# Kernel tuning notes

Measured on AMD Instinct MI355X. Metric: run time of the kernel, lower is better.

Reference implementation:

```python
import jax, jax.numpy as jnp
import numpy as np

H, N, CH, RANK = 512, 64, 1, 1
SEQ_L = 4096


def setup_inputs() -> dict:
    key = jax.random.key(0)
    k0, k1, k2, k3, k4 = jax.random.split(key, 5)
    # A = -exp(A_real) + i*A_imag  (real_transform='exp'); HiPPO-style imag init
    A_real = jnp.log(0.5 + jax.random.uniform(k0, (H, N), dtype=jnp.float32))
    A_imag = jnp.broadcast_to(np.pi * jnp.arange(N, dtype=jnp.float32), (H, N)).copy()
    # complex params stored as (..., 2) real/imag pairs (torch.view_as_real layout)
    B = (0.5 ** 0.5) * jax.random.normal(k1, (1, H, N, 2), dtype=jnp.float32)
    C = jax.random.normal(k2, (CH, H, N, 2), dtype=jnp.float32)
    P = (0.5 ** 0.5) * jax.random.normal(k3, (RANK, H, N, 2), dtype=jnp.float32)
    # dt = exp(inv_dt) log-uniform in [1e-3, 1e-1]  (dt_transform='exp')
    lo, hi = np.log(1e-3), np.log(1e-1)
    inv_dt = (lo + (hi - lo) * jax.random.uniform(k4, (H,), dtype=jnp.float32)).astype(jnp.float32)
    return {"A_real": A_real, "A_imag": A_imag, "B": B, "C": C, "P": P,
            "inv_dt": inv_dt, "L": SEQ_L}


def _c(x):
    # view_as_complex
    return x[..., 0] + 1j * x[..., 1]


def _s4_kernel(A_real, A_imag, B, C, P, inv_dt, L):
    dt = jnp.exp(inv_dt)                       # (H,)
    A = -jnp.exp(A_real) + 1j * A_imag          # (H, N) complex64
    Bc, Cc, Pc = _c(B), _c(C), _c(P)            # (1,H,N), (CH,H,N), (R,H,N)
    Q = jnp.conj(Pc)

    Lf = L // 2 + 1
    omega = jnp.exp(-2j * jnp.pi / L) ** jnp.arange(Lf)   # FFT nodes, (Lf,)
    z = 2 * (1 - omega) / (1 + omega)                      # bilinear-transform freqs

    A_dt = A * dt[:, None]                     # (H, N)
    Bcat = jnp.concatenate([Bc, Pc], axis=0)   # (1+R, H, N)
    Ccat = jnp.concatenate([Cc, Q], axis=0)    # (CH+R, H, N)
    v = Bcat[:, None] * Ccat[None]             # (1+R, CH+R, H, N)
    v = v * dt[:, None]

    # Cauchy kernel with implicit conjugate-pair symmetry:
    #   r[a,b,h,l] = sum_n v/(z - A_dt) + conj(v)/(z - conj(A_dt))
    denom = 1.0 / (z - A_dt[..., None])                    # (H, N, Lf)
    r = jnp.einsum('abhn,hnl->abhl', v, denom)
    denom_c = 1.0 / (z - jnp.conj(A_dt)[..., None])
    r = r + jnp.einsum('abhn,hnl->abhl', jnp.conj(v), denom_c)

    # rank-1 Woodbury correction
    k_f = r[:-1, :-1] - r[:-1, -1:] * r[-1:, :-1] / (1 + r[-1:, -1:])
    k_f = k_f * 2 / (1 + omega)

    k = jnp.fft.irfft(k_f, n=L)                # (1, CH, H, L) real
    k = k[..., :L]
    return k[-1]                               # k_B: (CH, H, L)


def reference(A_real, A_imag, B, C, P, inv_dt, L):
    return _s4_kernel(A_real, A_imag, B, C, P, inv_dt, L)
```

## Files before the change

kernel.cpp:

```cpp
#include <hip/hip_runtime.h>
#include <math.h>

namespace {
constexpr int kH = 512;
constexpr int kN = 64;
constexpr int kL = 4096;
constexpr int kM = 2048;
constexpr int kRec = 20;
constexpr int kThreads = 256;
constexpr int kFftThreads = 512;
constexpr float kPi = 3.14159265358979323846f;
}

__device__ __forceinline__ int lpad(int i) { return i + (i >> 4); }

__global__ __launch_bounds__(64)
void s4_prep(const float* __restrict__ A_real, const float* __restrict__ A_imag,
             const float* __restrict__ Bv, const float* __restrict__ Cv,
             const float* __restrict__ Pv, const float* __restrict__ inv_dt,
             float* __restrict__ cst)
{
    const int h = blockIdx.x;
    const int n = threadIdx.x;
    const int idx = h * kN + n;
    const float dt = expf(inv_dt[h]);
    const float ar = -expf(A_real[idx]) * dt;
    const float ai =  A_imag[idx] * dt;
    const float br = Bv[idx*2+0], bi = Bv[idx*2+1];
    const float cr = Cv[idx*2+0], ci = Cv[idx*2+1];
    const float pr = Pv[idx*2+0], pi = Pv[idx*2+1];
    const float v00r = (br*cr - bi*ci)*dt, v00i = (br*ci + bi*cr)*dt;
    const float v01r = (br*pr + bi*pi)*dt, v01i = (bi*pr - br*pi)*dt;
    const float v10r = (pr*cr - pi*ci)*dt, v10i = (pr*ci + pi*cr)*dt;
    const float v11r = (pr*pr + pi*pi)*dt;
    const float ar2 = ar*ar;
    const float C1  = ar2 + ai*ai;
    const float dd  = ar2 - ai*ai;

    float* r = cst + idx * kRec;
    r[0]  = ai;  r[1] = ar2;
    r[2]  = -2.f*C1*(v00r*ar + v00i*ai);  r[3]  = 2.f*(v00i*ai - v00r*ar);
    r[4]  = -4.f*v00r*dd - 8.f*v00i*ar*ai; r[5]  = -4.f*v00r;
    r[6]  = -2.f*C1*(v01r*ar + v01i*ai);  r[7]  = 2.f*(v01i*ai - v01r*ar);
    r[8]  = -4.f*v01r*dd - 8.f*v01i*ar*ai; r[9]  = -4.f*v01r;
    r[10] = -2.f*C1*(v10r*ar + v10i*ai);  r[11] = 2.f*(v10i*ai - v10r*ar);
    r[12] = -4.f*v10r*dd - 8.f*v10i*ar*ai; r[13] = -4.f*v10r;
    r[14] = -2.f*C1*(v11r*ar);            r[15] = -2.f*v11r*ar;
    r[16] = -4.f*v11r*dd;                 r[17] = -4.f*v11r;
    r[18] = 0.f; r[19] = 0.f;
}

__global__ __launch_bounds__(kThreads)
void s4_spectrum(const float* __restrict__ cst, float2* __restrict__ Xg)
{
    const int h   = blockIdx.x >> 2;
    const int q   = blockIdx.x & 3;
    const int tid = threadIdx.x;
    const int la  = q * 512 + tid;

    float tv[2], t2v[2], sv[2];
    #pragma unroll
    for (int b = 0; b < 2; ++b) {
        const int l = la + 256 * b;
        float sn, cn;
        sincosf((float)l * (kPi / (float)kL), &sn, &cn);
        tv[b]  = sn / cn;
        t2v[b] = 2.f * tv[b];
        sv[b]  = t2v[b] * t2v[b];
    }

    float A0[2][4] = {{0,0,0,0},{0,0,0,0}};
    float A1[2][4] = {{0,0,0,0},{0,0,0,0}};
    float B0[2][4] = {{0,0,0,0},{0,0,0,0}};
    float B1[2][4] = {{0,0,0,0},{0,0,0,0}};

    const float* rec = cst + (size_t)h * kN * kRec;
    #pragma unroll 1
    for (int n0 = 0; n0 < kN; n0 += 4) {
        float rr[4][18];
        #pragma unroll
        for (int j = 0; j < 4; ++j) {
            const float* r = rec + (n0 + j) * kRec;
            #pragma unroll
            for (int k = 0; k < 18; ++k) rr[j][k] = r[k];
        }
        #pragma unroll
        for (int j = 0; j < 4; ++j) {
            const float ai = rr[j][0], ar2 = rr[j][1];
            #pragma unroll
            for (int b = 0; b < 2; ++b) {
                const float w1 = t2v[b] - ai, w2 = t2v[b] + ai;
                const float m1 = fmaf(w1, w1, ar2), m2 = fmaf(w2, w2, ar2);
                const float invD = __builtin_amdgcn_rcpf(m1 * m2);
                #pragma unroll
                for (int p = 0; p < 4; ++p) {
                    A0[b][p] = fmaf(rr[j][2 + 4*p], invD, A0[b][p]);
                    A1[b][p] = fmaf(rr[j][3 + 4*p], invD, A1[b][p]);
                    B0[b][p] = fmaf(rr[j][4 + 4*p], invD, B0[b][p]);
                    B1[b][p] = fmaf(rr[j][5 + 4*p], invD, B1[b][p]);
                }
            }
        }
    }

    #pragma unroll
    for (int b = 0; b < 2; ++b) {
        const int l = la + 256 * b;
        const float t = tv[b], s = sv[b];
        const float s00r = fmaf(s, A1[b][0], A0[b][0]);
        const float s00i = t * fmaf(s, B1[b][0], B0[b][0]);
        const float s01r = fmaf(s, A1[b][1], A0[b][1]);
        const float s01i = t * fmaf(s, B1[b][1], B0[b][1]);
        const float s10r = fmaf(s, A1[b][2], A0[b][2]);
        const float s10i = t * fmaf(s, B1[b][2], B0[b][2]);
        const float s11r = fmaf(s, A1[b][3], A0[b][3]);
        const float s11i = t * fmaf(s, B1[b][3], B0[b][3]);
        const float nr = s01r*s10r - s01i*s10i;
        const float ni = s01r*s10i + s01i*s10r;
        const float dr = 1.f + s11r, di = s11i;
        const float qd = __builtin_amdgcn_rcpf(fmaf(dr, dr, di*di));
        const float wr = (nr*dr + ni*di) * qd;
        const float wi = (ni*dr - nr*di) * qd;
        const float gr = s00r - wr, gi = s00i - wi;
        Xg[h*kM + l] = make_float2(fmaf(-gi, t, gr), fmaf(gr, t, gi));
    }
}

__global__ __launch_bounds__(kFftThreads)
void s4_ifft(const float* __restrict__ Bv,
             const float* __restrict__ Cv,
             const float* __restrict__ inv_dt,
             float* __restrict__ out)
{
    __shared__ float2 W2[kM + kM / 16];
    __shared__ float2 TW[kM / 2 + kM / 32];
    __shared__ float  XnyqR;

    const int h   = blockIdx.x;
    const int tid = threadIdx.x;
    const float2* Xg = (const float2*)(out + (size_t)h * kL);

    if (tid < kN) {
        const int idx = h * kN + tid;
        const float dt = expf(inv_dt[h]);
        const float br = Bv[idx*2+0], bi = Bv[idx*2+1];
        const float cr = Cv[idx*2+0], ci = Cv[idx*2+1];
        float vr = (br*cr - bi*ci) * dt;
        #pragma unroll
        for (int off = 32; off > 0; off >>= 1) vr += __shfl_down(vr, off, 64);
        if (tid == 0) XnyqR = vr;
    }
    for (int j = tid; j < kM / 2; j += kFftThreads) {
        float s, c;
        sincosf((2.0f * kPi / (float)kM) * (float)j, &s, &c);
        TW[lpad(j)] = make_float2(c, s);
    }
    __syncthreads();

    for (int k = tid; k <= kM / 2; k += kFftThreads) {
        const float2 Xa = Xg[k];
        const float2 Xb = (k == 0) ? make_float2(XnyqR, 0.0f) : Xg[kM - k];
        const float Er = 0.5f * (Xa.x + Xb.x);
        const float Ei = 0.5f * (Xa.y - Xb.y);
        const float Dr = 0.5f * (Xa.x - Xb.x);
        const float Di = 0.5f * (Xa.y + Xb.y);
        float s, c;
        sincosf((2.0f * kPi / (float)kL) * (float)k, &s, &c);
        const float Or = c * Dr - s * Di;
        const float Oi = c * Di + s * Dr;
        const int rk = (int)(__brev((unsigned)k) >> 21);
        W2[lpad(rk)] = make_float2(Er - Oi, Ei + Or);
        if (k != 0 && k != kM / 2) {
            const int rmk = (int)(__brev((unsigned)(kM - k)) >> 21);
            W2[lpad(rmk)] = make_float2(Er + Oi, Or - Ei);
        }
    }
    __syncthreads();

    for (int hs = 1; hs < kM; hs <<= 1) {
        const int tw_stride = (kM / 2) / hs;
        for (int j = tid; j < kM / 2; j += kFftThreads) {
            const int pos = j & (hs - 1);
            const int grp = j / hs;
            const int i0  = grp * 2 * hs + pos;
            const int i1  = i0 + hs;
            const float2 tw = TW[lpad(pos * tw_stride)];
            const float2 a = W2[lpad(i0)];
            const float2 b = W2[lpad(i1)];
            const float tr = tw.x * b.x - tw.y * b.y;
            const float ti = tw.x * b.y + tw.y * b.x;
            W2[lpad(i0)] = make_float2(a.x + tr, a.y + ti);
            W2[lpad(i1)] = make_float2(a.x - tr, a.y - ti);
        }
        __syncthreads();
    }

    const float invM = 1.0f / (float)kM;
    float2* out2 = (float2*)(out + (size_t)h * kL);
    for (int n = tid; n < kM; n += kFftThreads) {
        const float2 zn = W2[lpad(n)];
        out2[n] = make_float2(zn.x * invM, zn.y * invM);
    }
}

extern "C" void kernel_launch(void* const* d_in, const int* in_sizes, int n_in,
                              void* d_out, int out_size, void* d_ws, size_t ws_size,
                              hipStream_t stream) {
    const float* A_real = (const float*)d_in[0];
    const float* A_imag = (const float*)d_in[1];
    const float* B      = (const float*)d_in[2];
    const float* C      = (const float*)d_in[3];
    const float* P      = (const float*)d_in[4];
    const float* inv_dt = (const float*)d_in[5];
    float* out = (float*)d_out;

    float* cst = (float*)d_ws;

    s4_prep<<<dim3(kH), dim3(64), 0, stream>>>(A_real, A_imag, B, C, P, inv_dt,
                                               cst);
    s4_spectrum<<<dim3(kH * 4), dim3(kThreads), 0, stream>>>(cst, (float2*)out);
    s4_ifft<<<dim3(kH), dim3(kFftThreads), 0, stream>>>(B, C, inv_dt, out);
}
```

Before: 125.3 us.

## Pack coefficient records in pairs and use packed FP32 FMA in spectrum loop

The prep kernel now interleaves the coefficient records of two adjacent state indices into one 40-float pair record. The spectrum kernel processes two states per iteration using 2-wide vector FMAs (v_pk_fma_f32 on CDNA), keeping dual-lane accumulators and summing the lanes at the end. The aim is to halve the issue count of the dominant FMA accumulation and let the loads be vectorized. The cost is more accumulator registers and a slightly different summation order.

Result: faster. 113.4 us (-9.5%).

```diff
diff --git a/kernel.cpp b/kernel.cpp
--- a/kernel.cpp
+++ b/kernel.cpp
@@ -6,13 +6,18 @@
 constexpr int kN = 64;
 constexpr int kL = 4096;
 constexpr int kM = 2048;
-constexpr int kRec = 20;
+constexpr int kPairRec = 40;
 constexpr int kThreads = 256;
 constexpr int kFftThreads = 512;
 constexpr float kPi = 3.14159265358979323846f;
 }
 
+typedef float v2f __attribute__((ext_vector_type(2)));
+
 __device__ __forceinline__ int lpad(int i) { return i + (i >> 4); }
+__device__ __forceinline__ v2f fma2(v2f a, v2f b, v2f c) {
+    return __builtin_elementwise_fma(a, b, c);
+}
 
 __global__ __launch_bounds__(64)
 void s4_prep(const float* __restrict__ A_real, const float* __restrict__ A_imag,
@@ -37,17 +42,21 @@
     const float C1  = ar2 + ai*ai;
     const float dd  = ar2 - ai*ai;
 
-    float* r = cst + idx * kRec;
-    r[0]  = ai;  r[1] = ar2;
-    r[2]  = -2.f*C1*(v00r*ar + v00i*ai);  r[3]  = 2.f*(v00i*ai - v00r*ar);
-    r[4]  = -4.f*v00r*dd - 8.f*v00i*ar*ai; r[5]  = -4.f*v00r;
-    r[6]  = -2.f*C1*(v01r*ar + v01i*ai);  r[7]  = 2.f*(v01i*ai - v01r*ar);
-    r[8]  = -4.f*v01r*dd - 8.f*v01i*ar*ai; r[9]  = -4.f*v01r;
-    r[10] = -2.f*C1*(v10r*ar + v10i*ai);  r[11] = 2.f*(v10i*ai - v10r*ar);
-    r[12] = -4.f*v10r*dd - 8.f*v10i*ar*ai; r[13] = -4.f*v10r;
-    r[14] = -2.f*C1*(v11r*ar);            r[15] = -2.f*v11r*ar;
-    r[16] = -4.f*v11r*dd;                 r[17] = -4.f*v11r;
-    r[18] = 0.f; r[19] = 0.f;
+    float co[16];
+    co[0]  = -2.f*C1*(v00r*ar + v00i*ai);   co[1]  = 2.f*(v00i*ai - v00r*ar);
+    co[2]  = -4.f*v00r*dd - 8.f*v00i*ar*ai; co[3]  = -4.f*v00r;
+    co[4]  = -2.f*C1*(v01r*ar + v01i*ai);   co[5]  = 2.f*(v01i*ai - v01r*ar);
+    co[6]  = -4.f*v01r*dd - 8.f*v01i*ar*ai; co[7]  = -4.f*v01r;
+    co[8]  = -2.f*C1*(v10r*ar + v10i*ai);   co[9]  = 2.f*(v10i*ai - v10r*ar);
+    co[10] = -4.f*v10r*dd - 8.f*v10i*ar*ai; co[11] = -4.f*v10r;
+    co[12] = -2.f*C1*(v11r*ar);             co[13] = -2.f*v11r*ar;
+    co[14] = -4.f*v11r*dd;                  co[15] = -4.f*v11r;
+
+    float* base = cst + ((size_t)h * (kN/2) + (n >> 1)) * kPairRec + (n & 1);
+    base[0] = ai;
+    base[2] = ar2;
+    #pragma unroll
+    for (int k = 0; k < 16; ++k) base[4 + 2*k] = co[k];
 }
 
 __global__ __launch_bounds__(kThreads)
@@ -58,47 +67,50 @@
     const int tid = threadIdx.x;
     const int la  = q * 512 + tid;
 
-    float tv[2], t2v[2], sv[2];
+    float tv[2], sv[2];
+    v2f t2p[2];
     #pragma unroll
     for (int b = 0; b < 2; ++b) {
         const int l = la + 256 * b;
         float sn, cn;
         sincosf((float)l * (kPi / (float)kL), &sn, &cn);
-        tv[b]  = sn / cn;
-        t2v[b] = 2.f * tv[b];
-        sv[b]  = t2v[b] * t2v[b];
-    }
-
-    float A0[2][4] = {{0,0,0,0},{0,0,0,0}};
-    float A1[2][4] = {{0,0,0,0},{0,0,0,0}};
-    float B0[2][4] = {{0,0,0,0},{0,0,0,0}};
-    float B1[2][4] = {{0,0,0,0},{0,0,0,0}};
-
-    const float* rec = cst + (size_t)h * kN * kRec;
-    #pragma unroll 1
-    for (int n0 = 0; n0 < kN; n0 += 4) {
-        float rr[4][18];
+        tv[b] = sn / cn;
+        const float t2 = 2.f * tv[b];
+        sv[b] = t2 * t2;
+        t2p[b] = (v2f){t2, t2};
+    }
+
+    v2f A0[2][4], A1[2][4], B0[2][4], B1[2][4];
+    #pragma unroll
+    for (int b = 0; b < 2; ++b)
         #pragma unroll
-        for (int j = 0; j < 4; ++j) {
-            const float* r = rec + (n0 + j) * kRec;
+        for (int p = 0; p < 4; ++p) {
+            A0[b][p] = (v2f){0.f, 0.f}; A1[b][p] = (v2f){0.f, 0.f};
+            B0[b][p] = (v2f){0.f, 0.f}; B1[b][p] = (v2f){0.f, 0.f};
+        }
+
+    const v2f* rec = (const v2f*)(cst + (size_t)h * (kN/2) * kPairRec);
+    #pragma unroll 2
+    for (int j = 0; j < kN/2; ++j) {
+        const v2f* r = rec + j * (kPairRec/2);
+        const v2f aip  = r[0];
+        const v2f ar2p = r[1];
+        #pragma unroll
+        for (int b = 0; b < 2; ++b) {
+            const v2f w1 = t2p[b] - aip;
+            const v2f w2 = t2p[b] + aip;
+            const v2f m1 = fma2(w1, w1, ar2p);
+            const v2f m2 = fma2(w2, w2, ar2p);
+            const v2f D  = m1 * m2;
+            v2f qv;
+            qv.x = __builtin_amdgcn_rcpf(D.x);
+            qv.y = __builtin_amdgcn_rcpf(D.y);
             #pragma unroll
-            for (int k = 0; k < 18; ++k) rr[j][k] = r[k];
-        }
-        #pragma unroll
-        for (int j = 0; j < 4; ++j) {
-            const float ai = rr[j][0], ar2 = rr[j][1];
-            #pragma unroll
-            for (int b = 0; b < 2; ++b) {
-                const float w1 = t2v[b] - ai, w2 = t2v[b] + ai;
-                const float m1 = fmaf(w1, w1, ar2), m2 = fmaf(w2, w2, ar2);
-                const float invD = __builtin_amdgcn_rcpf(m1 * m2);
-                #pragma unroll
-                for (int p = 0; p < 4; ++p) {
-                    A0[b][p] = fmaf(rr[j][2 + 4*p], invD, A0[b][p]);
-                    A1[b][p] = fmaf(rr[j][3 + 4*p], invD, A1[b][p]);
-                    B0[b][p] = fmaf(rr[j][4 + 4*p], invD, B0[b][p]);
-                    B1[b][p] = fmaf(rr[j][5 + 4*p], invD, B1[b][p]);
-                }
+            for (int p = 0; p < 4; ++p) {
+                A0[b][p] = fma2(r[2 + 4*p + 0], qv, A0[b][p]);
+                A1[b][p] = fma2(r[2 + 4*p + 1], qv, A1[b][p]);
+                B0[b][p] = fma2(r[2 + 4*p + 2], qv, B0[b][p]);
+                B1[b][p] = fma2(r[2 + 4*p + 3], qv, B1[b][p]);
             }
         }
     }
@@ -106,15 +118,20 @@
     #pragma unroll
     for (int b = 0; b < 2; ++b) {
         const int l = la + 256 * b;
-        const float t = tv[b], s = sv[b];
-        const float s00r = fmaf(s, A1[b][0], A0[b][0]);
-        const float s00i = t * fmaf(s, B1[b][0], B0[b][0]);
-        const float s01r = fmaf(s, A1[b][1], A0[b][1]);
-        const float s01i = t * fmaf(s, B1[b][1], B0[b][1]);
-        const float s10r = fmaf(s, A1[b][2], A0[b][2]);
-        const float s10i = t * fmaf(s, B1[b][2], B0[b][2]);
-        const float s11r = fmaf(s, A1[b][3], A0[b][3]);
-        const float s11i = t * fmaf(s, B1[b][3], B0[b][3]);
+        const float t = tv[b];
+        const v2f sp = (v2f){sv[b], sv[b]};
+        const v2f r00 = fma2(sp, A1[b][0], A0[b][0]);
+        const v2f i00 = fma2(sp, B1[b][0], B0[b][0]);
+        const v2f r01 = fma2(sp, A1[b][1], A0[b][1]);
+        const v2f i01 = fma2(sp, B1[b][1], B0[b][1]);
+        const v2f r10 = fma2(sp, A1[b][2], A0[b][2]);
+        const v2f i10 = fma2(sp, B1[b][2], B0[b][2]);
+        const v2f r11 = fma2(sp, A1[b][3], A0[b][3]);
+        const v2f i11 = fma2(sp, B1[b][3], B0[b][3]);
+        const float s00r = r00.x + r00.y, s00i = t * (i00.x + i00.y);
+        const float s01r = r01.x + r01.y, s01i = t * (i01.x + i01.y);
+        const float s10r = r10.x + r10.y, s10i = t * (i10.x + i10.y);
+        const float s11r = r11.x + r11.y, s11i = t * (i11.x + i11.y);
         const float nr = s01r*s10r - s01i*s10i;
         const float ni = s01r*s10i + s01i*s10r;
         const float dr = 1.f + s11r, di = s11i;
```
